# Kernel tuning notes

Hardware: AMD Instinct MI355X
Metric: run time of the kernel (lower is better)

Reference implementation:

```python
import jax, jax.numpy as jnp
import numpy as np

N_NODES = 100000
N_EDGES = 1600000
NODE_DIM = 64
EDGE_DIM = 32
HIDDEN = 128
OUT_DIM = 64


def setup_inputs() -> dict:
    key = jax.random.key(0)
    ks = jax.random.split(key, 6)
    x = jax.random.normal(ks[0], (N_NODES, NODE_DIM), dtype=jnp.float32)
    edge_attr = jax.random.normal(ks[1], (N_EDGES, EDGE_DIM), dtype=jnp.float32)
    in_dim = 2 * NODE_DIM + EDGE_DIM  # 160
    W1 = jax.random.normal(ks[2], (in_dim, HIDDEN), dtype=jnp.float32) * (1.0 / np.sqrt(in_dim))
    b1 = jnp.zeros((HIDDEN,), dtype=jnp.float32)
    W2 = jax.random.normal(ks[3], (HIDDEN, OUT_DIM), dtype=jnp.float32) * (1.0 / np.sqrt(HIDDEN))
    b2 = jnp.zeros((OUT_DIM,), dtype=jnp.float32)
    edge_index = jax.random.randint(ks[4], (2, N_EDGES), 0, N_NODES, dtype=jnp.int64)
    return {"x": x, "edge_attr": edge_attr, "W1": W1, "b1": b1, "W2": W2, "b2": b2,
            "edge_index": edge_index}


def reference(x, edge_attr, W1, b1, W2, b2, edge_index):
    src, tgt = edge_index[0], edge_index[1]
    # gather source/target node features, concat with edge features: [E, 2*node_dim+edge_dim]
    merged = jnp.concatenate([x[src], x[tgt], edge_attr], axis=1)
    h = jax.nn.relu(merged @ W1 + b1)   # [E, HIDDEN]
    return h @ W2 + b2                  # [E, OUT_DIM]
```

## Files before the change

kernel.cpp:

```cpp
#include <hip/hip_runtime.h>

#define E_TOTAL 1600000
#define ND 64
#define ED 32
#define IN_DIM 160
#define HID 128
#define OUTD 64

#define TM 128
#define A_STRIDE 168
#define H_STRIDE 136

typedef short v8s __attribute__((ext_vector_type(8)));
typedef float v4f __attribute__((ext_vector_type(4)));

__device__ __forceinline__ unsigned short f2bf(float f) {
    union { float f; unsigned u; } v; v.f = f;
    unsigned u = v.u;
    u += 0x7FFFu + ((u >> 16) & 1u);
    return (unsigned short)(u >> 16);
}

__global__ void prep_weights(const float* __restrict__ W1, const float* __restrict__ W2,
                             unsigned short* __restrict__ w1t, unsigned short* __restrict__ w2t) {
    int i = blockIdx.x * blockDim.x + threadIdx.x;
    if (i < IN_DIM * HID) {
        int n = i / IN_DIM, k = i % IN_DIM;
        w1t[i] = f2bf(W1[k * HID + n]);
    } else {
        int j = i - IN_DIM * HID;
        if (j < HID * OUTD) {
            int n = j / HID, k = j % HID;
            w2t[j] = f2bf(W2[k * OUTD + n]);
        }
    }
}

__global__ __launch_bounds__(256) void edge_mlp(
    const float* __restrict__ x, const float* __restrict__ ea,
    const float* __restrict__ b1, const float* __restrict__ b2,
    const int* __restrict__ eidx,
    const unsigned short* __restrict__ w1t, const unsigned short* __restrict__ w2t,
    float* __restrict__ out)
{
    __shared__ unsigned short Alds[TM * A_STRIDE];

    const int tid = threadIdx.x;
    const int e0 = blockIdx.x * TM;

    {
        const int p = tid >> 1;
        const int half = tid & 1;
        const int e = e0 + p;
        const int node = eidx[half * E_TOTAL + e];
        const float4* xr = (const float4*)(x + (long)node * ND);
        unsigned short* arow = &Alds[p * A_STRIDE + half * ND];
#pragma unroll
        for (int k = 0; k < 16; ++k) {
            float4 f = xr[k];
            ushort4 s; s.x = f2bf(f.x); s.y = f2bf(f.y); s.z = f2bf(f.z); s.w = f2bf(f.w);
            *(ushort4*)(arow + 4 * k) = s;
        }
        const float4* er = (const float4*)(ea + (long)e * ED + half * 16);
        unsigned short* arow2 = &Alds[p * A_STRIDE + 2 * ND + half * 16];
#pragma unroll
        for (int k = 0; k < 4; ++k) {
            float4 f = er[k];
            ushort4 s; s.x = f2bf(f.x); s.y = f2bf(f.y); s.z = f2bf(f.z); s.w = f2bf(f.w);
            *(ushort4*)(arow2 + 4 * k) = s;
        }
    }
    __syncthreads();

    const int w = tid >> 6;
    const int lane = tid & 63;
    const int q = lane >> 4;
    const int c = lane & 15;
    const int wr = w >> 1, wc = w & 1;

    v4f acc[4][4] = {};
#pragma unroll
    for (int kk = 0; kk < 5; ++kk) {
        const int kb = kk * 32 + q * 8;
        v8s a[4], b[4];
#pragma unroll
        for (int i = 0; i < 4; ++i)
            a[i] = *(const v8s*)&Alds[(wr * 64 + i * 16 + c) * A_STRIDE + kb];
#pragma unroll
        for (int j = 0; j < 4; ++j)
            b[j] = *(const v8s*)&w1t[(wc * 64 + j * 16 + c) * IN_DIM + kb];
#pragma unroll
        for (int i = 0; i < 4; ++i)
#pragma unroll
            for (int j = 0; j < 4; ++j)
                acc[i][j] = __builtin_amdgcn_mfma_f32_16x16x32_bf16(a[i], b[j], acc[i][j], 0, 0, 0);
    }
    __syncthreads();

#pragma unroll
    for (int j = 0; j < 4; ++j) {
        const int col = wc * 64 + j * 16 + c;
        const float bias = b1[col];
#pragma unroll
        for (int i = 0; i < 4; ++i) {
            const int rbase = wr * 64 + i * 16 + q * 4;
#pragma unroll
            for (int r = 0; r < 4; ++r) {
                float v = acc[i][j][r] + bias;
                v = v > 0.f ? v : 0.f;
                Alds[(rbase + r) * H_STRIDE + col] = f2bf(v);
            }
        }
    }
    __syncthreads();

    v4f acc2[4][2] = {};
#pragma unroll
    for (int kk = 0; kk < 4; ++kk) {
        const int kb = kk * 32 + q * 8;
        v8s a[4], b[2];
#pragma unroll
        for (int i = 0; i < 4; ++i)
            a[i] = *(const v8s*)&Alds[(wr * 64 + i * 16 + c) * H_STRIDE + kb];
#pragma unroll
        for (int j = 0; j < 2; ++j)
            b[j] = *(const v8s*)&w2t[(wc * 32 + j * 16 + c) * HID + kb];
#pragma unroll
        for (int i = 0; i < 4; ++i)
#pragma unroll
            for (int j = 0; j < 2; ++j)
                acc2[i][j] = __builtin_amdgcn_mfma_f32_16x16x32_bf16(a[i], b[j], acc2[i][j], 0, 0, 0);
    }

#pragma unroll
    for (int j = 0; j < 2; ++j) {
        const int o = wc * 32 + j * 16 + c;
        const float bias = b2[o];
#pragma unroll
        for (int i = 0; i < 4; ++i) {
            const int rbase = wr * 64 + i * 16 + q * 4;
#pragma unroll
            for (int r = 0; r < 4; ++r) {
                const long e = (long)e0 + rbase + r;
                out[e * OUTD + o] = acc2[i][j][r] + bias;
            }
        }
    }
}

extern "C" void kernel_launch(void* const* d_in, const int* in_sizes, int n_in,
                              void* d_out, int out_size, void* d_ws, size_t ws_size,
                              hipStream_t stream) {
    const float* x  = (const float*)d_in[0];
    const float* ea = (const float*)d_in[1];
    const float* W1 = (const float*)d_in[2];
    const float* b1 = (const float*)d_in[3];
    const float* W2 = (const float*)d_in[4];
    const float* b2 = (const float*)d_in[5];
    const int* eidx = (const int*)d_in[6];
    float* out = (float*)d_out;

    unsigned short* w1t = (unsigned short*)d_ws;
    unsigned short* w2t = w1t + IN_DIM * HID;

    prep_weights<<<(IN_DIM * HID + HID * OUTD + 255) / 256, 256, 0, stream>>>(W1, W2, w1t, w2t);
    edge_mlp<<<E_TOTAL / TM, 256, 0, stream>>>(x, ea, b1, b2, eidx, w1t, w2t, out);
}
```

Measured before the change: 767.4 us.

## Gather node features straight into MFMA registers and pre-convert x to bf16

Edge features and gathered node rows are now loaded directly from global memory into the MFMA A-operand registers, which removes the LDS staging buffer and its first barrier. When the workspace is large enough, a new prep kernel converts all of x to bf16 once, so each gather reads half the bytes and skips per-edge conversion. Weights are pre-swizzled into per-lane fragment order so the B loads are contiguous, and launch bounds ask for 4 blocks per CU. In exchange, node rows are now read in 16-byte pieces per lane, which can hurt coalescing, and the extra prep pass adds about 38 MB of traffic.

Result: faster. 735.1 us (-4.2%).

```diff
diff --git a/kernel.cpp b/kernel.cpp
--- a/kernel.cpp
+++ b/kernel.cpp
@@ -1,6 +1,7 @@
 #include <hip/hip_runtime.h>
 
 #define E_TOTAL 1600000
+#define N_NODES 100000
 #define ND 64
 #define ED 32
 #define IN_DIM 160
@@ -8,7 +9,6 @@
 #define OUTD 64
 
 #define TM 128
-#define A_STRIDE 168
 #define H_STRIDE 136
 
 typedef short v8s __attribute__((ext_vector_type(8)));
@@ -21,94 +21,100 @@
     return (unsigned short)(u >> 16);
 }
 
+__device__ __forceinline__ v8s cvt8(float4 f0, float4 f1) {
+    v8s r;
+    r[0] = (short)f2bf(f0.x); r[1] = (short)f2bf(f0.y);
+    r[2] = (short)f2bf(f0.z); r[3] = (short)f2bf(f0.w);
+    r[4] = (short)f2bf(f1.x); r[5] = (short)f2bf(f1.y);
+    r[6] = (short)f2bf(f1.z); r[7] = (short)f2bf(f1.w);
+    return r;
+}
+
+__global__ void prep_x(const float* __restrict__ x, unsigned short* __restrict__ xbf) {
+    int i = blockIdx.x * blockDim.x + threadIdx.x;
+    if (i < N_NODES * ND) xbf[i] = f2bf(x[i]);
+}
+
 __global__ void prep_weights(const float* __restrict__ W1, const float* __restrict__ W2,
-                             unsigned short* __restrict__ w1t, unsigned short* __restrict__ w2t) {
+                             unsigned short* __restrict__ w1f, unsigned short* __restrict__ w2f) {
     int i = blockIdx.x * blockDim.x + threadIdx.x;
     if (i < IN_DIM * HID) {
-        int n = i / IN_DIM, k = i % IN_DIM;
-        w1t[i] = f2bf(W1[k * HID + n]);
-    } else {
-        int j = i - IN_DIM * HID;
-        if (j < HID * OUTD) {
-            int n = j / HID, k = j % HID;
-            w2t[j] = f2bf(W2[k * OUTD + n]);
-        }
+        int t8 = i & 7, lane = (i >> 3) & 63, jk = i >> 9;
+        int kk = jk >> 3, jt = jk & 7, cc = lane & 15, qq = lane >> 4;
+        int n = jt * 16 + cc, k = kk * 32 + qq * 8 + t8;
+        w1f[i] = f2bf(W1[k * HID + n]);
+    } else if (i < IN_DIM * HID + HID * OUTD) {
+        int u = i - IN_DIM * HID;
+        int t8 = u & 7, lane = (u >> 3) & 63, jk = u >> 9;
+        int kk = jk >> 2, jt = jk & 3, cc = lane & 15, qq = lane >> 4;
+        int n = jt * 16 + cc, k = kk * 32 + qq * 8 + t8;
+        w2f[u] = f2bf(W2[k * OUTD + n]);
     }
 }
 
-__global__ __launch_bounds__(256) void edge_mlp(
-    const float* __restrict__ x, const float* __restrict__ ea,
+template<bool XBF>
+__global__ __launch_bounds__(256, 4) void edge_mlp(
+    const float* __restrict__ x, const unsigned short* __restrict__ xbf,
+    const float* __restrict__ ea,
     const float* __restrict__ b1, const float* __restrict__ b2,
     const int* __restrict__ eidx,
-    const unsigned short* __restrict__ w1t, const unsigned short* __restrict__ w2t,
+    const unsigned short* __restrict__ w1f, const unsigned short* __restrict__ w2f,
     float* __restrict__ out)
 {
-    __shared__ unsigned short Alds[TM * A_STRIDE];
+    __shared__ unsigned short h[TM * H_STRIDE];
 
-    const int tid = threadIdx.x;
+    const int tid = threadIdx.x, lane = tid & 63, w = tid >> 6;
+    const int wr = w >> 1, wc = w & 1, c = lane & 15, q = lane >> 4;
     const int e0 = blockIdx.x * TM;
 
-    {
-        const int p = tid >> 1;
-        const int half = tid & 1;
-        const int e = e0 + p;
-        const int node = eidx[half * E_TOTAL + e];
-        const float4* xr = (const float4*)(x + (long)node * ND);
-        unsigned short* arow = &Alds[p * A_STRIDE + half * ND];
+    int eRow[4], srcOff[4], tgtOff[4];
 #pragma unroll
-        for (int k = 0; k < 16; ++k) {
-            float4 f = xr[k];
-            ushort4 s; s.x = f2bf(f.x); s.y = f2bf(f.y); s.z = f2bf(f.z); s.w = f2bf(f.w);
-            *(ushort4*)(arow + 4 * k) = s;
-        }
-        const float4* er = (const float4*)(ea + (long)e * ED + half * 16);
-        unsigned short* arow2 = &Alds[p * A_STRIDE + 2 * ND + half * 16];
-#pragma unroll
-        for (int k = 0; k < 4; ++k) {
-            float4 f = er[k];
-            ushort4 s; s.x = f2bf(f.x); s.y = f2bf(f.y); s.z = f2bf(f.z); s.w = f2bf(f.w);
-            *(ushort4*)(arow2 + 4 * k) = s;
-        }
+    for (int i = 0; i < 4; ++i) {
+        eRow[i] = e0 + wr * 64 + i * 16 + c;
+        srcOff[i] = eidx[eRow[i]] * ND;
+        tgtOff[i] = eidx[E_TOTAL + eRow[i]] * ND;
     }
-    __syncthreads();
-
-    const int w = tid >> 6;
-    const int lane = tid & 63;
-    const int q = lane >> 4;
-    const int c = lane & 15;
-    const int wr = w >> 1, wc = w & 1;
 
     v4f acc[4][4] = {};
 #pragma unroll
     for (int kk = 0; kk < 5; ++kk) {
-        const int kb = kk * 32 + q * 8;
-        v8s a[4], b[4];
+        v8s a[4];
 #pragma unroll
-        for (int i = 0; i < 4; ++i)
-            a[i] = *(const v8s*)&Alds[(wr * 64 + i * 16 + c) * A_STRIDE + kb];
+        for (int i = 0; i < 4; ++i) {
+            if (kk < 4) {
+                const int off = (kk < 2 ? srcOff[i] : tgtOff[i]) + (kk & 1) * 32 + q * 8;
+                if (XBF) {
+                    a[i] = *(const v8s*)(xbf + off);
+                } else {
+                    const float4* p = (const float4*)(x + off);
+                    a[i] = cvt8(p[0], p[1]);
+                }
+            } else {
+                const float4* p = (const float4*)(ea + (long)eRow[i] * ED + q * 8);
+                a[i] = cvt8(p[0], p[1]);
+            }
+        }
+        v8s b[4];
 #pragma unroll
         for (int j = 0; j < 4; ++j)
-            b[j] = *(const v8s*)&w1t[(wc * 64 + j * 16 + c) * IN_DIM + kb];
+            b[j] = *(const v8s*)(w1f + ((kk * 8 + wc * 4 + j) * 64 + lane) * 8);
 #pragma unroll
         for (int i = 0; i < 4; ++i)
 #pragma unroll
             for (int j = 0; j < 4; ++j)
                 acc[i][j] = __builtin_amdgcn_mfma_f32_16x16x32_bf16(a[i], b[j], acc[i][j], 0, 0, 0);
     }
-    __syncthreads();
 
 #pragma unroll
     for (int j = 0; j < 4; ++j) {
-        const int col = wc * 64 + j * 16 + c;
-        const float bias = b1[col];
+        const float bias = b1[wc * 64 + j * 16 + c];
 #pragma unroll
         for (int i = 0; i < 4; ++i) {
-            const int rbase = wr * 64 + i * 16 + q * 4;
 #pragma unroll
             for (int r = 0; r < 4; ++r) {
                 float v = acc[i][j][r] + bias;
                 v = v > 0.f ? v : 0.f;
-                Alds[(rbase + r) * H_STRIDE + col] = f2bf(v);
+                h[(wr * 64 + i * 16 + q * 4 + r) * H_STRIDE + wc * 64 + j * 16 + c] = f2bf(v);
             }
         }
     }
@@ -117,14 +123,14 @@
     v4f acc2[4][2] = {};
 #pragma unroll
     for (int kk = 0; kk < 4; ++kk) {
-        const int kb = kk * 32 + q * 8;
-        v8s a[4], b[2];
+        v8s a[4];
 #pragma unroll
         for (int i = 0; i < 4; ++i)
-            a[i] = *(const v8s*)&Alds[(wr * 64 + i * 16 + c) * H_STRIDE + kb];
+            a[i] = *(const v8s*)(h + (wr * 64 + i * 16 + c) * H_STRIDE + kk * 32 + q * 8);
+        v8s b[2];
 #pragma unroll
         for (int j = 0; j < 2; ++j)
-            b[j] = *(const v8s*)&w2t[(wc * 32 + j * 16 + c) * HID + kb];
+            b[j] = *(const v8s*)(w2f + ((kk * 4 + wc * 2 + j) * 64 + lane) * 8);
 #pragma unroll
         for (int i = 0; i < 4; ++i)
 #pragma unroll
@@ -134,15 +140,13 @@
 
 #pragma unroll
     for (int j = 0; j < 2; ++j) {
-        const int o = wc * 32 + j * 16 + c;
-        const float bias = b2[o];
+        const float bias = b2[wc * 32 + j * 16 + c];
 #pragma unroll
         for (int i = 0; i < 4; ++i) {
-            const int rbase = wr * 64 + i * 16 + q * 4;
 #pragma unroll
             for (int r = 0; r < 4; ++r) {
-                const long e = (long)e0 + rbase + r;
-                out[e * OUTD + o] = acc2[i][j][r] + bias;
+                const long e = (long)e0 + wr * 64 + i * 16 + q * 4 + r;
+                out[e * OUTD + wc * 32 + j * 16 + c] = acc2[i][j][r] + bias;
             }
         }
     }
@@ -160,9 +164,21 @@
     const int* eidx = (const int*)d_in[6];
     float* out = (float*)d_out;
 
-    unsigned short* w1t = (unsigned short*)d_ws;
-    unsigned short* w2t = w1t + IN_DIM * HID;
+    const size_t nx = (size_t)N_NODES * ND;
+    const size_t need = (nx + IN_DIM * HID + HID * OUTD) * 2;
+    const int nw = IN_DIM * HID + HID * OUTD;
 
-    prep_weights<<<(IN_DIM * HID + HID * OUTD + 255) / 256, 256, 0, stream>>>(W1, W2, w1t, w2t);
-    edge_mlp<<<E_TOTAL / TM, 256, 0, stream>>>(x, ea, b1, b2, eidx, w1t, w2t, out);
+    if (ws_size >= need) {
+        unsigned short* xbf = (unsigned short*)d_ws;
+        unsigned short* w1f = xbf + nx;
+        unsigned short* w2f = w1f + IN_DIM * HID;
+        prep_x<<<(int)((nx + 255) / 256), 256, 0, stream>>>(x, xbf);
+        prep_weights<<<(nw + 255) / 256, 256, 0, stream>>>(W1, W2, w1f, w2f);
+        edge_mlp<true><<<E_TOTAL / TM, 256, 0, stream>>>(x, xbf, ea, b1, b2, eidx, w1f, w2f, out);
+    } else {
+        unsigned short* w1f = (unsigned short*)d_ws;
+        unsigned short* w2f = w1f + IN_DIM * HID;
+        prep_weights<<<(nw + 255) / 256, 256, 0, stream>>>(W1, W2, w1f, w2f);
+        edge_mlp<false><<<E_TOTAL / TM, 256, 0, stream>>>(x, nullptr, ea, b1, b2, eidx, w1f, w2f, out);
+    }
 }
```
